# Kernel tuning notes

Hardware: AMD Instinct MI355X
Metric: run time of the kernel (lower is better)

Reference implementation:

```python
import jax, jax.numpy as jnp
import numpy as np

B, C, H_IMG, W_IMG = 1, 32, 192, 192
WS = 16            # window_size / group_size
SS = 32            # sample_size = 2*window_size (unfold kernel)
PAD = (SS - WS) // 2
HEADS = 4
HD = C // HEADS
SCALE = HD ** -0.5
TOPK = WS * 16     # 256


def _group(x):
    # 'b c (nh sh)(nw sw) -> (b nh nw) (sh sw) c'
    b, c, H, W = x.shape
    nh, nw = H // WS, W // WS
    return x.reshape(b, c, nh, WS, nw, WS).transpose(0, 2, 4, 3, 5, 1).reshape(b * nh * nw, WS * WS, c)


def _unfold_sample(x):
    # F.unfold(kernel=SS, stride=WS, pad=PAD) then 'b (c k0 k1) l -> (b l) (k0 k1) c'
    b, c = x.shape[:2]
    p = jax.lax.conv_general_dilated_patches(x, (SS, SS), (WS, WS), ((PAD, PAD), (PAD, PAD)))
    nh, nw = p.shape[2], p.shape[3]
    return p.reshape(b, c, SS * SS, nh * nw).transpose(0, 3, 2, 1).reshape(b * nh * nw, SS * SS, c)


def _rope(x):
    # interleaved rotary over the token axis (lucidrains rotate_queries_or_keys)
    n, d = x.shape[-2], x.shape[-1]
    half = d // 2
    freqs = 1.0 / (10000.0 ** (jnp.arange(0, d, 2, dtype=jnp.float32) / d))
    ang = jnp.arange(n, dtype=jnp.float32)[:, None] * freqs[None]          # (n, half)
    cos = jnp.repeat(jnp.cos(ang), 2, axis=-1)
    sin = jnp.repeat(jnp.sin(ang), 2, axis=-1)
    xp = x.reshape(x.shape[:-1] + (half, 2))
    rot = jnp.stack([-xp[..., 1], xp[..., 0]], axis=-1).reshape(x.shape)
    return x * cos + rot * sin


def _l2norm(x):
    return x / jnp.maximum(jnp.linalg.norm(x, axis=-1, keepdims=True), 1e-12)


def _diff(x):
    b, c, H, W = x.shape
    down = jax.image.resize(x, (b, c, H // 2, W // 2), 'bilinear')
    up = jax.image.resize(down, (b, c, H, W), 'bilinear')
    return jnp.abs(x - up).sum(1)  # (b, H, W)


def _alloc(var, budget, maximum, iters=4):
    # deterministic variant of the iterative proportional budget allocation
    rest = jnp.ones_like(var)
    for _ in range(iters):
        var_p = var * (rest < maximum)
        prop = var_p / jnp.maximum(var_p.sum(-1, keepdims=True), 1e-12)
        new_rest = jnp.clip(rest + jnp.round(prop * budget[:, None]), 0.0, maximum)
        budget = jnp.maximum(budget - (new_rest - rest).sum(-1), 0.0)
        rest = new_rest
    return rest


def _calc_graph(x):
    # local-sampling graph (sampling_method=0); computed under no_grad in torch
    Xd = _diff(x)
    b = x.shape[0]
    nh, nw = H_IMG // WS, W_IMG // WS
    Xd_g = Xd.reshape(b, nh, WS, nw, WS).transpose(0, 1, 3, 2, 4).reshape(b * nh * nw, WS * WS)
    Xg = _group(x)            # (b_, m, c)
    Ys = _unfold_sample(x)    # (b_, n, c)
    D = jnp.einsum('bmc,bnc->bmn', _l2norm(Xg), _l2norm(Ys))
    idx = jnp.argsort(-D, axis=-1)  # descending sort indices
    b_, m, n = idx.shape
    budget = jnp.full((b_,), float((TOPK - 1) * m), jnp.float32)
    mask_array = _alloc(Xd_g, budget, float(n))              # (b_, m)
    mask = jnp.arange(n, dtype=jnp.float32)[None, None] > mask_array[..., None]
    inv = jnp.argsort(idx, axis=-1)
    # graph[b,m,idx[k]] = ~mask[b,m,k]; idx is a permutation per row
    return jnp.take_along_axis(~mask, inv, axis=-1)          # (b_, m, n) bool, True = keep


def _forward(x, Wg, bg, Ws, bs, Wp, bp, Wc, bc, gamma, beta):
    graph = _calc_graph(jax.lax.stop_gradient(x))
    x_grp = _group(x)                                        # (b_, m, c)
    b_, m, c = x_grp.shape
    # proj_group: 1x1 Conv1d == linear over channels; 'b (h c) n -> b h n c'
    x1 = (x_grp @ Wg.T + bg).reshape(b_, m, HEADS, HD).transpose(0, 2, 1, 3)
    # proj_sample: 1x1 Conv2d to 2*dim, then unfold-sample
    y = jnp.einsum('bchw,oc->bohw', x, Ws) + bs[None, :, None, None]
    ys = _unfold_sample(y)                                   # (b_, n, 2c)
    n = ys.shape[1]
    x2 = ys[..., :C].reshape(b_, n, HEADS, HD).transpose(0, 2, 1, 3)
    feat = ys[..., C:].reshape(b_, n, HEADS, HD).transpose(0, 2, 1, 3)
    q = _rope(x1)
    k = _rope(x2)
    sim = jnp.einsum('bhmc,bhnc->bhmn', _l2norm(q), _l2norm(k)) - 100.0 * (~graph)[:, None]
    attn = jax.nn.softmax(sim * SCALE, axis=-1)
    out = jnp.einsum('bhmn,bhnc->bhmc', attn, feat).transpose(0, 2, 1, 3).reshape(b_, m, C)
    out = out @ Wp.T + bp
    # '(b nh nw)(sh sw) c -> b c (nh sh)(nw sw)'
    nh, nw = H_IMG // WS, W_IMG // WS
    img = out.reshape(B, nh, nw, WS, WS, C).transpose(0, 5, 1, 3, 2, 4).reshape(B, C, H_IMG, W_IMG)
    conv = jax.lax.conv_general_dilated(img, Wc, (1, 1), 'SAME',
                                        dimension_numbers=('NCHW', 'OIHW', 'NCHW')) + bc[None, :, None, None]
    cl = conv.transpose(0, 2, 3, 1)
    mu = cl.mean(-1, keepdims=True)
    var = cl.var(-1, keepdims=True)
    normed = (cl - mu) / jnp.sqrt(var + 1e-5) * gamma + beta
    return img + normed.transpose(0, 3, 1, 2)


def setup_inputs() -> dict:
    key = jax.random.key(0)
    ks = jax.random.split(key, 8)
    s = 1.0 / np.sqrt(C)
    return {
        'x': jax.random.normal(ks[0], (B, C, H_IMG, W_IMG), jnp.float32),
        'Wg': jax.random.normal(ks[1], (C, C), jnp.float32) * s,
        'bg': jnp.zeros((C,), jnp.float32),
        'Ws': jax.random.normal(ks[2], (2 * C, C), jnp.float32) * s,
        'bs': jnp.zeros((2 * C,), jnp.float32),
        'Wp': jax.random.normal(ks[3], (C, C), jnp.float32) * s,
        'bp': jnp.zeros((C,), jnp.float32),
        'Wc': jax.random.normal(ks[4], (C, C, 3, 3), jnp.float32) * (1.0 / np.sqrt(C * 9)),
        'bc': jnp.zeros((C,), jnp.float32),
        'gamma': jnp.ones((C,), jnp.float32),
        'beta': jnp.zeros((C,), jnp.float32),
    }


def reference(x, Wg, bg, Ws, bs, Wp, bp, Wc, bc, gamma, beta):
    return _forward(x, Wg, bg, Ws, bs, Wp, bp, Wc, bc, gamma, beta)
```

## Files before the change

### kernel.cpp

```cpp
#include <hip/hip_runtime.h>
#include <hip/hip_fp16.h>

namespace {

constexpr int CH = 32;
constexpr int HIMG = 192, WIMG = 192, NPIX = HIMG * WIMG;
constexpr int WSZ = 16, PADS = 8;
constexpr int NHW = 12, NWIN = 144;
constexpr int MQ = 256, NKEY = 1024;
constexpr int NHEAD = 4, HDIM = 8;
constexpr float SCL = 0.35355339059327373f;

typedef _Float16 half_t;
typedef __attribute__((ext_vector_type(2))) _Float16 h2;

__device__ __forceinline__ h2 mkh2(float v) { half_t h = (half_t)v; h2 r = {h, h}; return r; }

__device__ __forceinline__ unsigned sortable(float d) {
  unsigned b = __float_as_uint(d);
  if ((b << 1) == 0u) b = 0u;
  return (b & 0x80000000u) ? ~b : (b | 0x80000000u);
}

__global__ __launch_bounds__(256) void k_prep(const float* __restrict__ x,
                                              const float* __restrict__ Ws,
                                              const float* __restrict__ bs,
                                              float* __restrict__ y_px,
                                              float* __restrict__ xn) {
  __shared__ float xs[CH][4];
  int t = threadIdx.x;
  int pix0 = blockIdx.x * 4;
  if (t < CH * 4) {
    int c = t >> 2, ps = t & 3;
    xs[c][ps] = x[c * NPIX + pix0 + ps];
  }
  __syncthreads();
  int o = t & 63, pp = t >> 6;
  int pix = pix0 + pp;
  float wr[CH];
  const float4* wf = (const float4*)(Ws + o * CH);
#pragma unroll
  for (int r = 0; r < 8; ++r) {
    float4 v = wf[r];
    wr[4 * r] = v.x; wr[4 * r + 1] = v.y; wr[4 * r + 2] = v.z; wr[4 * r + 3] = v.w;
  }
  float a = bs[o];
#pragma unroll
  for (int c = 0; c < CH; ++c) a += wr[c] * xs[c][pp];
  y_px[pix * 64 + o] = a;
  float val = xs[o & 31][pp];
  float sq = val * val;
#pragma unroll
  for (int msk = 16; msk >= 1; msk >>= 1) sq += __shfl_xor(sq, msk, 32);
  float inv = 1.f / fmaxf(sqrtf(sq), 1e-12f);
  if (o < 32) xn[pix * CH + o] = val * inv;
}

__device__ __forceinline__ void down_w(int i, float w[4]) {
  w[0] = 0.125f; w[1] = 0.375f; w[2] = 0.375f; w[3] = 0.125f;
  if (i == 0)  { w[0] = 0.f;            w[1] = 0.75f / 1.75f; w[2] = 0.75f / 1.75f; w[3] = 0.25f / 1.75f; }
  if (i == 95) { w[0] = 0.25f / 1.75f;  w[1] = 0.75f / 1.75f; w[2] = 0.75f / 1.75f; w[3] = 0.f; }
}

__global__ __launch_bounds__(256) void k_down(const float* __restrict__ x,
                                              float* __restrict__ down) {
  int idx = blockIdx.x * 256 + threadIdx.x;
  if (idx >= CH * 96 * 96) return;
  int c = idx / (96 * 96);
  int r = (idx / 96) % 96;
  int q = idx % 96;
  float wr[4], wc[4];
  down_w(r, wr); down_w(q, wc);
  const float* xc = x + c * NPIX;
  float acc = 0.f;
#pragma unroll
  for (int a = 0; a < 4; ++a) {
    int rr = 2 * r - 1 + a;
    rr = rr < 0 ? 0 : (rr > HIMG - 1 ? HIMG - 1 : rr);
    float rowacc = 0.f;
#pragma unroll
    for (int bb = 0; bb < 4; ++bb) {
      int cc = 2 * q - 1 + bb;
      cc = cc < 0 ? 0 : (cc > WIMG - 1 ? WIMG - 1 : cc);
      rowacc += wc[bb] * xc[rr * WIMG + cc];
    }
    acc += wr[a] * rowacc;
  }
  down[idx] = acc;
}

__device__ __forceinline__ void up_taps(int i, int& j0, int& j1, float& w0, float& w1) {
  if (i == 0)        { j0 = 0;  j1 = 0;  w0 = 1.f;   w1 = 0.f;   return; }
  if (i == HIMG - 1) { j0 = 95; j1 = 95; w0 = 1.f;   w1 = 0.f;   return; }
  int tt = i >> 1;
  if ((i & 1) == 0)  { j0 = tt - 1; j1 = tt;     w0 = 0.25f; w1 = 0.75f; }
  else               { j0 = tt;     j1 = tt + 1; w0 = 0.75f; w1 = 0.25f; }
}

__global__ __launch_bounds__(256) void k_updiff(const float* __restrict__ x,
                                                const float* __restrict__ down,
                                                float* __restrict__ Xd) {
  int pix = blockIdx.x * 256 + threadIdx.x;
  int hh = pix / WIMG, wp = pix % WIMG;
  int r0, r1, c0, c1; float rw0, rw1, cw0, cw1;
  up_taps(hh, r0, r1, rw0, rw1);
  up_taps(wp, c0, c1, cw0, cw1);
  float s = 0.f;
  for (int c = 0; c < CH; ++c) {
    const float* d = down + c * 96 * 96;
    float up = rw0 * (cw0 * d[r0 * 96 + c0] + cw1 * d[r0 * 96 + c1]) +
               rw1 * (cw0 * d[r1 * 96 + c0] + cw1 * d[r1 * 96 + c1]);
    s += fabsf(x[c * NPIX + pix] - up);
  }
  Xd[pix] = s;
}

__global__ __launch_bounds__(256) void k_alloc(const float* __restrict__ Xd,
                                               int* __restrict__ Kall) {
  __shared__ float red[256];
  int win = blockIdx.x, t = threadIdx.x;
  int wh = win / NHW, ww = win % NHW;
  int pix = (wh * WSZ + (t >> 4)) * WIMG + ww * WSZ + (t & 15);
  float var = Xd[pix];
  float rest = 1.f;
  float budget = 65280.f;
  for (int it = 0; it < 4; ++it) {
    float vp = (rest < 1024.f) ? var : 0.f;
    red[t] = vp;
    __syncthreads();
    for (int s = 128; s > 0; s >>= 1) { if (t < s) red[t] += red[t + s]; __syncthreads(); }
    float sum = red[0];
    __syncthreads();
    float prop = vp / fmaxf(sum, 1e-12f);
    float nr = fminf(fmaxf(rest + rintf(prop * budget), 0.f), 1024.f);
    red[t] = nr - rest;
    __syncthreads();
    for (int s = 128; s > 0; s >>= 1) { if (t < s) red[t] += red[t + s]; __syncthreads(); }
    float dsum = red[0];
    __syncthreads();
    budget = fmaxf(budget - dsum, 0.f);
    rest = nr;
  }
  int K = (int)rest + 1;
  Kall[win * MQ + t] = K > 1024 ? 1024 : K;
}

__global__ __launch_bounds__(256) void k_qn(const float* __restrict__ x,
                                            const float* __restrict__ Wg,
                                            const float* __restrict__ bg,
                                            float* __restrict__ qn) {
  __shared__ float w[CH * CH];
  __shared__ float b[CH];
  int t = threadIdx.x;
  for (int i = t; i < CH * CH; i += 256) w[i] = Wg[i];
  if (t < CH) b[t] = bg[t];
  __syncthreads();
  int win = blockIdx.x;
  int wh = win / NHW, ww = win % NHW;
  int m = t;
  int pix = (wh * WSZ + (m >> 4)) * WIMG + ww * WSZ + (m & 15);
  float o[CH];
#pragma unroll
  for (int oc = 0; oc < CH; ++oc) o[oc] = b[oc];
  for (int c = 0; c < CH; ++c) {
    float xv = x[c * NPIX + pix];
#pragma unroll
    for (int oc = 0; oc < CH; ++oc) o[oc] += w[oc * CH + c] * xv;
  }
  const float invf[4] = {1.f, 0.1f, 0.01f, 0.001f};
  float pos = (float)m;
#pragma unroll
  for (int h = 0; h < NHEAD; ++h) {
#pragma unroll
    for (int p = 0; p < 4; ++p) {
      float ang = pos * invf[p];
      float cs = cosf(ang), sn = sinf(ang);
      int i0 = h * HDIM + 2 * p;
      float a0 = o[i0], a1 = o[i0 + 1];
      o[i0]     = a0 * cs - a1 * sn;
      o[i0 + 1] = a1 * cs + a0 * sn;
    }
  }
#pragma unroll
  for (int h = 0; h < NHEAD; ++h) {
    float ss = 0.f;
#pragma unroll
    for (int d = 0; d < HDIM; ++d) { float v = o[h * HDIM + d]; ss += v * v; }
    float den = fmaxf(sqrtf(ss), 1e-12f);
#pragma unroll
    for (int d = 0; d < HDIM; ++d)
      qn[(win * MQ + m) * CH + h * HDIM + d] = o[h * HDIM + d] / den;
  }
}

#define ACC4(A, Y) { float4 _a = (A); acc += _a.x*(Y).x; acc += _a.y*(Y).y; acc += _a.z*(Y).z; acc += _a.w*(Y).w; }

__global__ __launch_bounds__(512, 4) void k_graph(const float* __restrict__ xn,
                                                  const int* __restrict__ Kall,
                                                  unsigned* __restrict__ graph) {
  constexpr int QPB = 8;
  __shared__ __align__(16) float qloc[QPB][CH];
  __shared__ unsigned ubuf[QPB][NKEY];
  __shared__ __align__(16) unsigned hist[QPB][256];
  int win = blockIdx.x >> 5;
  int qg  = blockIdx.x & 31;
  int wh = win / NHW, ww = win % NHW;
  int t = threadIdx.x;
  if (t < QPB * CH) {
    int qi = t >> 5, c = t & 31;
    int m = qg * QPB + qi;
    int pix = (wh * WSZ + (m >> 4)) * WIMG + ww * WSZ + (m & 15);
    qloc[qi][c] = xn[pix * CH + c];
  }
  __syncthreads();
#pragma unroll 1
  for (int kk = 0; kk < 2; ++kk) {
    int j = kk * 512 + t;
    int k0 = j >> 5, k1 = j & 31;
    int py = wh * WSZ - PADS + k0, px = ww * WSZ - PADS + k1;
    bool inb = (py >= 0) && (py < HIMG) && (px >= 0) && (px < WIMG);
    const float4* s4 = (const float4*)(xn + (py * WIMG + px) * CH);
    float accq[QPB];
#pragma unroll
    for (int q = 0; q < QPB; ++q) accq[q] = 0.f;
#pragma unroll 1
    for (int half = 0; half < 2; ++half) {
      float4 y0, y1, y2, y3;
      if (inb) {
        y0 = s4[half * 4 + 0]; y1 = s4[half * 4 + 1];
        y2 = s4[half * 4 + 2]; y3 = s4[half * 4 + 3];
      } else {
        y0 = y1 = y2 = y3 = make_float4(0.f, 0.f, 0.f, 0.f);
      }
#pragma unroll
      for (int q = 0; q < QPB; ++q) {
        const float4* qf = (const float4*)qloc[q] + half * 4;
        float acc = 0.f;
        ACC4(qf[0], y0); ACC4(qf[1], y1); ACC4(qf[2], y2); ACC4(qf[3], y3);
        accq[q] += acc;
      }
    }
#pragma unroll
    for (int q = 0; q < QPB; ++q) ubuf[q][j] = sortable(accq[q]);
  }
  __syncthreads();
  int w = t >> 6, l = t & 63;
  int m = qg * QPB + w;
  int K = Kall[win * MQ + m];
  unsigned v[16];
#pragma unroll
  for (int k = 0; k < 16; ++k) v[k] = ubuf[w][k * 64 + l];
  unsigned pref = 0;
  int remK = K;
  int shift = 24;
  unsigned ustar = 0;
  int quota = 0;
  for (int pass = 0; pass < 4; ++pass) {
    *(uint4*)&hist[w][l * 4] = make_uint4(0u, 0u, 0u, 0u);
    __asm__ volatile("s_waitcnt lgkmcnt(0)" ::: "memory");
#pragma unroll
    for (int k = 0; k < 16; ++k) {
      unsigned u = v[k];
      bool ok = (pass == 0) || ((u >> ((shift + 8) & 31)) == pref);
      if (ok) atomicAdd(&hist[w][(u >> shift) & 255u], 1u);
    }
    __asm__ volatile("s_waitcnt lgkmcnt(0)" ::: "memory");
    unsigned c0 = hist[w][l * 4 + 0], c1 = hist[w][l * 4 + 1];
    unsigned c2 = hist[w][l * 4 + 2], c3 = hist[w][l * 4 + 3];
    unsigned s3 = c3, s2 = c3 + c2, s1 = s2 + c1, s0 = s1 + c0;
    unsigned I = s0;
#pragma unroll
    for (int off = 1; off < 64; off <<= 1) {
      unsigned tv = __shfl_down(I, off);
      if (l + off < 64) I += tv;
    }
    unsigned E = I - s0;
    int bin = -1, newrem = 0;
    bool early = false;
    {
      int sb, sb1;
      sb = (int)(s3 + E); sb1 = (int)E;
      if (sb >= remK && sb1 < remK) { bin = l * 4 + 3; newrem = remK - sb1; early = (sb == remK); }
      sb = (int)(s2 + E); sb1 = (int)(s3 + E);
      if (sb >= remK && sb1 < remK) { bin = l * 4 + 2; newrem = remK - sb1; early = (sb == remK); }
      sb = (int)(s1 + E); sb1 = (int)(s2 + E);
      if (sb >= remK && sb1 < remK) { bin = l * 4 + 1; newrem = remK - sb1; early = (sb == remK); }
      sb = (int)(s0 + E); sb1 = (int)(s1 + E);
      if (sb >= remK && sb1 < remK) { bin = l * 4 + 0; newrem = remK - sb1; early = (sb == remK); }
    }
    unsigned long long bal = __ballot(bin >= 0);
    int src = __ffsll((long long)bal) - 1;
    int pk = newrem | (bin << 11) | (early ? (1 << 20) : 0);
    pk = __shfl(pk, src);
    pref = (pref << 8) | (unsigned)((pk >> 11) & 255);
    remK = pk & 0x7FF;
    if (((pk >> 20) & 1) || pass == 3) { ustar = pref << shift; quota = remK; break; }
    shift -= 8;
  }
  unsigned row32 = (unsigned)(win * MQ + m) * 32u;
  int running = 0;
#pragma unroll
  for (int k = 0; k < 16; ++k) {
    unsigned u = v[k];
    bool eq = (u == ustar);
    unsigned long long beq = __ballot(eq);
    int before = running + (int)__popcll(beq & ((1ull << l) - 1ull));
    bool keep = (u > ustar) || (eq && before < quota);
    running += (int)__popcll(beq);
    unsigned long long kb = __ballot(keep);
    if (l == 0) {
      graph[row32 + 2 * k]     = (unsigned)kb;
      graph[row32 + 2 * k + 1] = (unsigned)(kb >> 32);
    }
  }
}

#define MERGEA(MSK) {                                              \
  float mo = __shfl_xor(mrun, MSK);                                \
  float lo = __shfl_xor(lrun, MSK);                                \
  float b0 = __shfl_xor(__builtin_bit_cast(float, a0), MSK);       \
  float b1 = __shfl_xor(__builtin_bit_cast(float, a1), MSK);       \
  float b2 = __shfl_xor(__builtin_bit_cast(float, a2), MSK);       \
  float b3 = __shfl_xor(__builtin_bit_cast(float, a3), MSK);       \
  float mn = fmaxf(mrun, mo);                                      \
  float c1 = __expf(mrun - mn), c2 = __expf(mo - mn);              \
  lrun = lrun * c1 + lo * c2;                                      \
  h2 c1h = mkh2(c1), c2h = mkh2(c2);                               \
  a0 = a0 * c1h + __builtin_bit_cast(h2, b0) * c2h;                \
  a1 = a1 * c1h + __builtin_bit_cast(h2, b1) * c2h;                \
  a2 = a2 * c1h + __builtin_bit_cast(h2, b2) * c2h;                \
  a3 = a3 * c1h + __builtin_bit_cast(h2, b3) * c2h;                \
  mrun = mn; }

__global__ __launch_bounds__(256, 4) void k_attn(const float* __restrict__ qn,
                                                 const float* __restrict__ y_px,
                                                 const unsigned* __restrict__ graph,
                                                 float* __restrict__ att) {
  __shared__ uint4 knp[NKEY];
  __shared__ uint4 fvp[NKEY];
  int bid = blockIdx.x;
  int qq  = bid & 3;
  int h   = (bid >> 2) & 3;
  int win = bid >> 4;
  int wh = win / NHW, ww = win % NHW;
  int t = threadIdx.x;
  const float invf[4] = {1.f, 0.1f, 0.01f, 0.001f};
#pragma unroll
  for (int r = 0; r < 4; ++r) {
    int j = r * 256 + t;
    int k0 = j >> 5, k1 = j & 31;
    int py = wh * WSZ - PADS + k0, px = ww * WSZ - PADS + k1;
    bool inb = (py >= 0) && (py < HIMG) && (px >= 0) && (px < WIMG);
    float kv[8], fw[8];
    if (inb) {
      const float* src = y_px + (py * WIMG + px) * 64 + h * HDIM;
      const float4* a4 = (const float4*)src;
      const float4* b4 = (const float4*)(src + 32);
      float4 a0 = a4[0], a1 = a4[1], b0 = b4[0], b1 = b4[1];
      kv[0]=a0.x; kv[1]=a0.y; kv[2]=a0.z; kv[3]=a0.w;
      kv[4]=a1.x; kv[5]=a1.y; kv[6]=a1.z; kv[7]=a1.w;
      fw[0]=b0.x; fw[1]=b0.y; fw[2]=b0.z; fw[3]=b0.w;
      fw[4]=b1.x; fw[5]=b1.y; fw[6]=b1.z; fw[7]=b1.w;
    } else {
#pragma unroll
      for (int d = 0; d < 8; ++d) { kv[d] = 0.f; fw[d] = 0.f; }
    }
    float ro[8];
    float posj = (float)j;
#pragma unroll
    for (int p = 0; p < 4; ++p) {
      float ang = posj * invf[p];
      float cs = cosf(ang), sn = sinf(ang);
      ro[2 * p]     = kv[2 * p] * cs - kv[2 * p + 1] * sn;
      ro[2 * p + 1] = kv[2 * p + 1] * cs + kv[2 * p] * sn;
    }
    float ss = 0.f;
#pragma unroll
    for (int d = 0; d < 8; ++d) ss += ro[d] * ro[d];
    float iv = 1.f / fmaxf(sqrtf(ss), 1e-12f);
    union { uint4 u; h2 v[4]; } ku, fu;
#pragma unroll
    for (int p = 0; p < 4; ++p) {
      h2 kk = { (half_t)(ro[2*p] * iv), (half_t)(ro[2*p+1] * iv) };
      h2 ff = { (half_t)fw[2*p], (half_t)fw[2*p+1] };
      ku.v[p] = kk; fu.v[p] = ff;
    }
    knp[j] = ku.u;
    fvp[j] = fu.u;
  }
  __syncthreads();
  int s = t & 3, ql = t >> 2;
  int m = qq * 64 + ql;
  const float* qp = qn + (win * MQ + m) * CH + h * HDIM;
  h2 q0 = { (half_t)qp[0], (half_t)qp[1] };
  h2 q1 = { (half_t)qp[2], (half_t)qp[3] };
  h2 q2 = { (half_t)qp[4], (half_t)qp[5] };
  h2 q3 = { (half_t)qp[6], (half_t)qp[7] };
  const unsigned* gr = graph + (size_t)(win * MQ + m) * 32 + s * 8;
  float mrun = -1e30f, lrun = 0.f;
  h2 a0 = {0,0}, a1 = {0,0}, a2 = {0,0}, a3 = {0,0};
  int jbase = s * 256;
  for (int w8 = 0; w8 < 8; ++w8) {
    unsigned bits = gr[w8];
    while (bits) {
      int bb = __ffs(bits) - 1;
      bits &= bits - 1;
      int j = jbase + w8 * 32 + bb;
      uint4 kv = knp[j];
      float sd = __builtin_amdgcn_fdot2(q0, __builtin_bit_cast(h2, kv.x), 0.f, false);
      sd = __builtin_amdgcn_fdot2(q1, __builtin_bit_cast(h2, kv.y), sd, false);
      sd = __builtin_amdgcn_fdot2(q2, __builtin_bit_cast(h2, kv.z), sd, false);
      sd = __builtin_amdgcn_fdot2(q3, __builtin_bit_cast(h2, kv.w), sd, false);
      sd *= SCL;
      uint4 fw = fvp[j];
      if (sd <= mrun) {
        float pw = __expf(sd - mrun);
        lrun += pw;
        h2 ph = mkh2(pw);
        a0 += __builtin_bit_cast(h2, fw.x) * ph;
        a1 += __builtin_bit_cast(h2, fw.y) * ph;
        a2 += __builtin_bit_cast(h2, fw.z) * ph;
        a3 += __builtin_bit_cast(h2, fw.w) * ph;
      } else {
        float corr = __expf(mrun - sd);
        lrun = lrun * corr + 1.f;
        h2 ch = mkh2(corr);
        a0 = a0 * ch + __builtin_bit_cast(h2, fw.x);
        a1 = a1 * ch + __builtin_bit_cast(h2, fw.y);
        a2 = a2 * ch + __builtin_bit_cast(h2, fw.z);
        a3 = a3 * ch + __builtin_bit_cast(h2, fw.w);
        mrun = sd;
      }
    }
  }
  MERGEA(1);
  MERGEA(2);
  float invl = 1.f / lrun;
  h2 sel;
  if (s == 0) sel = a0; else if (s == 1) sel = a1; else if (s == 2) sel = a2; else sel = a3;
  float* op = att + (size_t)(win * MQ + m) * CH + h * HDIM + s * 2;
  op[0] = (float)sel.x * invl;
  op[1] = (float)sel.y * invl;
}

__global__ __launch_bounds__(256) void k_img(const float* __restrict__ att,
                                             const float* __restrict__ Wp,
                                             const float* __restrict__ bp,
                                             float* __restrict__ img) {
  __shared__ float w[CH * CH];
  __shared__ float b[CH];
  int t = threadIdx.x;
  for (int i = t; i < CH * CH; i += 256) w[i] = Wp[i];
  if (t < CH) b[t] = bp[t];
  __syncthreads();
  int gid = blockIdx.x * 256 + t;
  int win = gid >> 8, m = gid & 255;
  int wh = win / NHW, ww = win % NHW;
  int pix = (wh * WSZ + (m >> 4)) * WIMG + ww * WSZ + (m & 15);
  float a[CH];
#pragma unroll
  for (int c = 0; c < CH; ++c) a[c] = att[(size_t)gid * CH + c];
  for (int oc = 0; oc < CH; ++oc) {
    float acc = b[oc];
#pragma unroll
    for (int c = 0; c < CH; ++c) acc += w[oc * CH + c] * a[c];
    img[oc * NPIX + pix] = acc;
  }
}

#define CACC(W, I0) { o[I0] += (W).x * xv; o[I0+1] += (W).y * xv; o[I0+2] += (W).z * xv; o[I0+3] += (W).w * xv; }

__global__ __launch_bounds__(256) void k_convln(const float* __restrict__ img,
                                                const float* __restrict__ Wc,
                                                const float* __restrict__ bc,
                                                const float* __restrict__ gamma,
                                                const float* __restrict__ beta,
                                                float* __restrict__ out) {
  __shared__ float tile[CH][10][18];
  __shared__ __align__(16) float wt[288][CH];
  __shared__ float red[128][2][2];
  int t = threadIdx.x;
  int by = (blockIdx.x / 12) * 8, bx = (blockIdx.x % 12) * 16;
  for (int i = t; i < 288 * CH; i += 256) {
    int oc = i & 31, icd = i >> 5;
    wt[icd][oc] = Wc[oc * 288 + icd];
  }
  for (int i = t; i < CH * 10 * 18; i += 256) {
    int c = i / 180; int rr = (i % 180) / 18; int cl = i % 18;
    int gy = by + rr - 1, gx = bx + cl - 1;
    tile[c][rr][cl] = (gy >= 0 && gy < HIMG && gx >= 0 && gx < WIMG)
                          ? img[c * NPIX + gy * WIMG + gx] : 0.f;
  }
  __syncthreads();
  int g = __builtin_amdgcn_readfirstlane((t >> 7) & 1);
  int p = t & 127;
  int r = p >> 4, c = p & 15;
  int ocb = g * 16;
  float o[16];
#pragma unroll
  for (int k = 0; k < 16; ++k) o[k] = bc[ocb + k];
  for (int ic = 0; ic < CH; ++ic) {
#pragma unroll
    for (int dy = 0; dy < 3; ++dy) {
#pragma unroll
      for (int dx = 0; dx < 3; ++dx) {
        float xv = tile[ic][r + dy][c + dx];
        const float4* wv = (const float4*)&wt[ic * 9 + dy * 3 + dx][ocb];
        float4 w0 = wv[0], w1 = wv[1], w2 = wv[2], w3 = wv[3];
        CACC(w0, 0); CACC(w1, 4); CACC(w2, 8); CACC(w3, 12);
      }
    }
  }
  float s1 = 0.f, s2 = 0.f;
#pragma unroll
  for (int k = 0; k < 16; ++k) { s1 += o[k]; s2 += o[k] * o[k]; }
  red[p][g][0] = s1; red[p][g][1] = s2;
  __syncthreads();
  float t1 = red[p][g ^ 1][0], t2 = red[p][g ^ 1][1];
  float mu = (s1 + t1) * (1.f / 32.f);
  float ex2 = (s2 + t2) * (1.f / 32.f);
  float var = ex2 - mu * mu;
  float inv = 1.f / sqrtf(var + 1e-5f);
  int pix = (by + r) * WIMG + bx + c;
#pragma unroll
  for (int k = 0; k < 16; ++k) {
    int oc = ocb + k;
    out[oc * NPIX + pix] = tile[oc][r + 1][c + 1] + (o[k] - mu) * inv * gamma[oc] + beta[oc];
  }
}

}

extern "C" void kernel_launch(void* const* d_in, const int* in_sizes, int n_in,
                              void* d_out, int out_size, void* d_ws, size_t ws_size,
                              hipStream_t stream) {
  const float* x     = (const float*)d_in[0];
  const float* Wg    = (const float*)d_in[1];
  const float* bg    = (const float*)d_in[2];
  const float* Ws    = (const float*)d_in[3];
  const float* bs    = (const float*)d_in[4];
  const float* Wp    = (const float*)d_in[5];
  const float* bp    = (const float*)d_in[6];
  const float* Wc    = (const float*)d_in[7];
  const float* bc    = (const float*)d_in[8];
  const float* gamma = (const float*)d_in[9];
  const float* beta  = (const float*)d_in[10];
  float* out = (float*)d_out;
  float* ws = (float*)d_ws;

  float* y_px = ws;
  float* xn   = y_px + 2359296;
  float* down = xn + 1179648;
  float* Xd   = down + 294912;
  float* qn   = Xd + 36864;
  float* att  = qn + 1179648;
  float* img  = att + 1179648;
  int* Kall   = (int*)(img + 1179648);
  unsigned* graph = (unsigned*)(Kall + 36864);
  if (ws_size < (size_t)8626176 * 4) return;

  k_prep<<<NPIX / 4, 256, 0, stream>>>(x, Ws, bs, y_px, xn);
  k_down<<<(CH * 96 * 96) / 256, 256, 0, stream>>>(x, down);
  k_updiff<<<NPIX / 256, 256, 0, stream>>>(x, down, Xd);
  k_alloc<<<NWIN, 256, 0, stream>>>(Xd, Kall);
  k_qn<<<NWIN, 256, 0, stream>>>(x, Wg, bg, qn);
  k_graph<<<NWIN * 32, 512, 0, stream>>>(xn, Kall, graph);
  k_attn<<<NWIN * NHEAD * 4, 256, 0, stream>>>(qn, y_px, graph, att);
  k_img<<<NPIX / 256, 256, 0, stream>>>(att, Wp, bp, img);
  k_convln<<<288, 256, 0, stream>>>(img, Wc, bc, gamma, beta, out);
}
```

Before: 351.7 us.

## Rework prep, qn, graph and img kernels for more parallelism and packed math

k_prep now processes 16 pixels per block, so each thread reuses its cached weights across four pixels, and it writes the L2-normalised features as float4. k_qn splits the output channels across two blocks per window, doubling the grid and halving register pressure. k_graph switches the similarity dot products to packed v_pk_fma_f32, skips the loads and math for out-of-bounds keys, and packs the radix histogram into 16-bit counters to halve its LDS footprint. k_img splits output channels across wavefronts, with vectorised loads of activations and weights. These changes target low occupancy and instruction count across several kernels, at the cost of more blocks and inline assembly.

After: 336.1 us. -4.4%, faster.

```diff
diff --git a/kernel.cpp b/kernel.cpp
--- a/kernel.cpp
+++ b/kernel.cpp
@@ -13,8 +13,15 @@
 
 typedef _Float16 half_t;
 typedef __attribute__((ext_vector_type(2))) _Float16 h2;
+typedef __attribute__((ext_vector_type(2))) float f32x2;
 
 __device__ __forceinline__ h2 mkh2(float v) { half_t h = (half_t)v; h2 r = {h, h}; return r; }
+
+__device__ __forceinline__ f32x2 pkfma(f32x2 a, f32x2 b, f32x2 c) {
+  f32x2 d;
+  asm("v_pk_fma_f32 %0, %1, %2, %3" : "=v"(d) : "v"(a), "v"(b), "v"(c));
+  return d;
+}
 
 __device__ __forceinline__ unsigned sortable(float d) {
   unsigned b = __float_as_uint(d);
@@ -27,16 +34,15 @@
                                               const float* __restrict__ bs,
                                               float* __restrict__ y_px,
                                               float* __restrict__ xn) {
-  __shared__ float xs[CH][4];
+  __shared__ float xs[CH][16];
   int t = threadIdx.x;
-  int pix0 = blockIdx.x * 4;
-  if (t < CH * 4) {
-    int c = t >> 2, ps = t & 3;
-    xs[c][ps] = x[c * NPIX + pix0 + ps];
-  }
-  __syncthreads();
-  int o = t & 63, pp = t >> 6;
-  int pix = pix0 + pp;
+  int pix0 = blockIdx.x * 16;
+  for (int i = t; i < CH * 16; i += 256) {
+    int c = i >> 4, p = i & 15;
+    xs[c][p] = x[c * NPIX + pix0 + p];
+  }
+  __syncthreads();
+  int o = t & 63, pg = t >> 6;
   float wr[CH];
   const float4* wf = (const float4*)(Ws + o * CH);
 #pragma unroll
@@ -44,16 +50,26 @@
     float4 v = wf[r];
     wr[4 * r] = v.x; wr[4 * r + 1] = v.y; wr[4 * r + 2] = v.z; wr[4 * r + 3] = v.w;
   }
-  float a = bs[o];
-#pragma unroll
-  for (int c = 0; c < CH; ++c) a += wr[c] * xs[c][pp];
-  y_px[pix * 64 + o] = a;
-  float val = xs[o & 31][pp];
-  float sq = val * val;
-#pragma unroll
-  for (int msk = 16; msk >= 1; msk >>= 1) sq += __shfl_xor(sq, msk, 32);
-  float inv = 1.f / fmaxf(sqrtf(sq), 1e-12f);
-  if (o < 32) xn[pix * CH + o] = val * inv;
+  float bo = bs[o];
+#pragma unroll
+  for (int pp = 0; pp < 4; ++pp) {
+    int p = pg * 4 + pp;
+    float a = bo;
+#pragma unroll
+    for (int c = 0; c < CH; ++c) a += wr[c] * xs[c][p];
+    y_px[(pix0 + p) * 64 + o] = a;
+  }
+  if (t < 128) {
+    int p = t >> 3, c8 = (t & 7) * 4;
+    float v0 = xs[c8][p], v1 = xs[c8 + 1][p], v2 = xs[c8 + 2][p], v3 = xs[c8 + 3][p];
+    float ss = v0 * v0 + v1 * v1 + v2 * v2 + v3 * v3;
+    ss += __shfl_xor(ss, 1);
+    ss += __shfl_xor(ss, 2);
+    ss += __shfl_xor(ss, 4);
+    float inv = 1.f / fmaxf(sqrtf(ss), 1e-12f);
+    float4 outv = make_float4(v0 * inv, v1 * inv, v2 * inv, v3 * inv);
+    *(float4*)(xn + (pix0 + p) * CH + c8) = outv;
+  }
 }
 
 __device__ __forceinline__ void down_w(int i, float w[4]) {
@@ -149,51 +165,50 @@
                                             const float* __restrict__ Wg,
                                             const float* __restrict__ bg,
                                             float* __restrict__ qn) {
-  __shared__ float w[CH * CH];
-  __shared__ float b[CH];
+  __shared__ float w[16 * CH];
+  __shared__ float b[16];
+  int bid = blockIdx.x;
+  int win = bid >> 1, g = bid & 1;
   int t = threadIdx.x;
-  for (int i = t; i < CH * CH; i += 256) w[i] = Wg[i];
-  if (t < CH) b[t] = bg[t];
-  __syncthreads();
-  int win = blockIdx.x;
+  for (int i = t; i < 16 * CH; i += 256) w[i] = Wg[g * 16 * CH + i];
+  if (t < 16) b[t] = bg[g * 16 + t];
+  __syncthreads();
   int wh = win / NHW, ww = win % NHW;
   int m = t;
   int pix = (wh * WSZ + (m >> 4)) * WIMG + ww * WSZ + (m & 15);
-  float o[CH];
-#pragma unroll
-  for (int oc = 0; oc < CH; ++oc) o[oc] = b[oc];
+  float o[16];
+#pragma unroll
+  for (int k = 0; k < 16; ++k) o[k] = b[k];
   for (int c = 0; c < CH; ++c) {
     float xv = x[c * NPIX + pix];
 #pragma unroll
-    for (int oc = 0; oc < CH; ++oc) o[oc] += w[oc * CH + c] * xv;
+    for (int k = 0; k < 16; ++k) o[k] += w[k * CH + c] * xv;
   }
   const float invf[4] = {1.f, 0.1f, 0.01f, 0.001f};
   float pos = (float)m;
 #pragma unroll
-  for (int h = 0; h < NHEAD; ++h) {
+  for (int lh = 0; lh < 2; ++lh) {
 #pragma unroll
     for (int p = 0; p < 4; ++p) {
       float ang = pos * invf[p];
       float cs = cosf(ang), sn = sinf(ang);
-      int i0 = h * HDIM + 2 * p;
+      int i0 = lh * 8 + 2 * p;
       float a0 = o[i0], a1 = o[i0 + 1];
       o[i0]     = a0 * cs - a1 * sn;
       o[i0 + 1] = a1 * cs + a0 * sn;
     }
   }
 #pragma unroll
-  for (int h = 0; h < NHEAD; ++h) {
+  for (int lh = 0; lh < 2; ++lh) {
     float ss = 0.f;
 #pragma unroll
-    for (int d = 0; d < HDIM; ++d) { float v = o[h * HDIM + d]; ss += v * v; }
+    for (int d = 0; d < 8; ++d) { float v = o[lh * 8 + d]; ss += v * v; }
     float den = fmaxf(sqrtf(ss), 1e-12f);
 #pragma unroll
-    for (int d = 0; d < HDIM; ++d)
-      qn[(win * MQ + m) * CH + h * HDIM + d] = o[h * HDIM + d] / den;
-  }
-}
-
-#define ACC4(A, Y) { float4 _a = (A); acc += _a.x*(Y).x; acc += _a.y*(Y).y; acc += _a.z*(Y).z; acc += _a.w*(Y).w; }
+    for (int d = 0; d < 8; ++d)
+      qn[(win * MQ + m) * CH + g * 16 + lh * 8 + d] = o[lh * 8 + d] / den;
+  }
+}
 
 __global__ __launch_bounds__(512, 4) void k_graph(const float* __restrict__ xn,
                                                   const int* __restrict__ Kall,
@@ -201,7 +216,7 @@
   constexpr int QPB = 8;
   __shared__ __align__(16) float qloc[QPB][CH];
   __shared__ unsigned ubuf[QPB][NKEY];
-  __shared__ __align__(16) unsigned hist[QPB][256];
+  __shared__ __align__(8) unsigned hist[QPB][128];
   int win = blockIdx.x >> 5;
   int qg  = blockIdx.x & 31;
   int wh = win / NHW, ww = win % NHW;
@@ -219,29 +234,31 @@
     int k0 = j >> 5, k1 = j & 31;
     int py = wh * WSZ - PADS + k0, px = ww * WSZ - PADS + k1;
     bool inb = (py >= 0) && (py < HIMG) && (px >= 0) && (px < WIMG);
-    const float4* s4 = (const float4*)(xn + (py * WIMG + px) * CH);
-    float accq[QPB];
-#pragma unroll
-    for (int q = 0; q < QPB; ++q) accq[q] = 0.f;
+    f32x2 acc2[QPB];
+#pragma unroll
+    for (int q = 0; q < QPB; ++q) acc2[q] = (f32x2){0.f, 0.f};
+    if (inb) {
+      const float4* s4 = (const float4*)(xn + (py * WIMG + px) * CH);
 #pragma unroll 1
-    for (int half = 0; half < 2; ++half) {
-      float4 y0, y1, y2, y3;
-      if (inb) {
-        y0 = s4[half * 4 + 0]; y1 = s4[half * 4 + 1];
-        y2 = s4[half * 4 + 2]; y3 = s4[half * 4 + 3];
-      } else {
-        y0 = y1 = y2 = y3 = make_float4(0.f, 0.f, 0.f, 0.f);
+      for (int half = 0; half < 2; ++half) {
+        union { float4 v4[4]; f32x2 v2[8]; } Y;
+#pragma unroll
+        for (int r = 0; r < 4; ++r) Y.v4[r] = s4[half * 4 + r];
+#pragma unroll
+        for (int c4 = 0; c4 < 4; ++c4) {
+          f32x2 y0 = Y.v2[2 * c4], y1 = Y.v2[2 * c4 + 1];
+#pragma unroll
+          for (int q = 0; q < QPB; ++q) {
+            float4 qv = ((const float4*)qloc[q])[half * 4 + c4];
+            f32x2 qa = {qv.x, qv.y}, qb = {qv.z, qv.w};
+            acc2[q] = pkfma(qa, y0, acc2[q]);
+            acc2[q] = pkfma(qb, y1, acc2[q]);
+          }
+        }
       }
-#pragma unroll
-      for (int q = 0; q < QPB; ++q) {
-        const float4* qf = (const float4*)qloc[q] + half * 4;
-        float acc = 0.f;
-        ACC4(qf[0], y0); ACC4(qf[1], y1); ACC4(qf[2], y2); ACC4(qf[3], y3);
-        accq[q] += acc;
-      }
-    }
-#pragma unroll
-    for (int q = 0; q < QPB; ++q) ubuf[q][j] = sortable(accq[q]);
+    }
+#pragma unroll
+    for (int q = 0; q < QPB; ++q) ubuf[q][j] = sortable(acc2[q].x + acc2[q].y);
   }
   __syncthreads();
   int w = t >> 6, l = t & 63;
@@ -256,17 +273,21 @@
   unsigned ustar = 0;
   int quota = 0;
   for (int pass = 0; pass < 4; ++pass) {
-    *(uint4*)&hist[w][l * 4] = make_uint4(0u, 0u, 0u, 0u);
+    *(uint2*)&hist[w][l * 2] = make_uint2(0u, 0u);
     __asm__ volatile("s_waitcnt lgkmcnt(0)" ::: "memory");
 #pragma unroll
     for (int k = 0; k < 16; ++k) {
       unsigned u = v[k];
       bool ok = (pass == 0) || ((u >> ((shift + 8) & 31)) == pref);
-      if (ok) atomicAdd(&hist[w][(u >> shift) & 255u], 1u);
+      if (ok) {
+        unsigned bin = (u >> shift) & 255u;
+        atomicAdd(&hist[w][bin >> 1], 1u << ((bin & 1) << 4));
+      }
     }
     __asm__ volatile("s_waitcnt lgkmcnt(0)" ::: "memory");
-    unsigned c0 = hist[w][l * 4 + 0], c1 = hist[w][l * 4 + 1];
-    unsigned c2 = hist[w][l * 4 + 2], c3 = hist[w][l * 4 + 3];
+    uint2 hw = *(const uint2*)&hist[w][l * 2];
+    unsigned c0 = hw.x & 0xFFFFu, c1 = hw.x >> 16;
+    unsigned c2 = hw.y & 0xFFFFu, c3 = hw.y >> 16;
     unsigned s3 = c3, s2 = c3 + c2, s1 = s2 + c1, s0 = s1 + c0;
     unsigned I = s0;
 #pragma unroll
@@ -447,23 +468,31 @@
                                              const float* __restrict__ Wp,
                                              const float* __restrict__ bp,
                                              float* __restrict__ img) {
-  __shared__ float w[CH * CH];
+  __shared__ __align__(16) float w[CH * CH];
   __shared__ float b[CH];
   int t = threadIdx.x;
   for (int i = t; i < CH * CH; i += 256) w[i] = Wp[i];
   if (t < CH) b[t] = bp[t];
   __syncthreads();
-  int gid = blockIdx.x * 256 + t;
-  int win = gid >> 8, m = gid & 255;
+  int g = t >> 6, lane = t & 63;
+  int gq = blockIdx.x * 64 + lane;
+  int win = gq >> 8, m = gq & 255;
   int wh = win / NHW, ww = win % NHW;
   int pix = (wh * WSZ + (m >> 4)) * WIMG + ww * WSZ + (m & 15);
-  float a[CH];
-#pragma unroll
-  for (int c = 0; c < CH; ++c) a[c] = att[(size_t)gid * CH + c];
-  for (int oc = 0; oc < CH; ++oc) {
+  union { float4 v4[8]; float f[CH]; } a;
+  const float4* ap = (const float4*)(att + (size_t)gq * CH);
+#pragma unroll
+  for (int r = 0; r < 8; ++r) a.v4[r] = ap[r];
+#pragma unroll
+  for (int k = 0; k < 8; ++k) {
+    int oc = g * 8 + k;
     float acc = b[oc];
-#pragma unroll
-    for (int c = 0; c < CH; ++c) acc += w[oc * CH + c] * a[c];
+    const float4* wv = (const float4*)&w[oc * CH];
+#pragma unroll
+    for (int c4 = 0; c4 < 8; ++c4) {
+      float4 wq = wv[c4];
+      acc += wq.x * a.f[4*c4] + wq.y * a.f[4*c4+1] + wq.z * a.f[4*c4+2] + wq.w * a.f[4*c4+3];
+    }
     img[oc * NPIX + pix] = acc;
   }
 }
@@ -559,13 +588,13 @@
   unsigned* graph = (unsigned*)(Kall + 36864);
   if (ws_size < (size_t)8626176 * 4) return;
 
-  k_prep<<<NPIX / 4, 256, 0, stream>>>(x, Ws, bs, y_px, xn);
+  k_prep<<<NPIX / 16, 256, 0, stream>>>(x, Ws, bs, y_px, xn);
   k_down<<<(CH * 96 * 96) / 256, 256, 0, stream>>>(x, down);
   k_updiff<<<NPIX / 256, 256, 0, stream>>>(x, down, Xd);
   k_alloc<<<NWIN, 256, 0, stream>>>(Xd, Kall);
-  k_qn<<<NWIN, 256, 0, stream>>>(x, Wg, bg, qn);
+  k_qn<<<NWIN * 2, 256, 0, stream>>>(x, Wg, bg, qn);
   k_graph<<<NWIN * 32, 512, 0, stream>>>(xn, Kall, graph);
   k_attn<<<NWIN * NHEAD * 4, 256, 0, stream>>>(qn, y_px, graph, att);
-  k_img<<<NPIX / 256, 256, 0, stream>>>(att, Wp, bp, img);
+  k_img<<<NPIX / 64, 256, 0, stream>>>(att, Wp, bp, img);
   k_convln<<<288, 256, 0, stream>>>(img, Wc, bc, gamma, beta, out);
 }
```
